# Kernel optimization log

Hardware: AMD Instinct MI355X
Metric: run time of the kernel (lower is better)

The kernel has to match this reference:

```python
import jax, jax.numpy as jnp
import numpy as np

B, C, H, W = 8, 256, 64, 64   # batch, num_hiddens, spatial
N, D = 1024, 256              # n_embed, embedding_dim
TEMP = 1.0                    # temp_init


def setup_inputs() -> dict:
    key = jax.random.key(0)
    k1, k2, k3 = jax.random.split(key, 3)
    z = jax.random.normal(k1, (B, C, H, W), dtype=jnp.float32)
    # 1x1 conv == per-pixel linear: weight [n_embed, num_hiddens], bias [n_embed]
    proj_w = jax.random.normal(k2, (N, C), dtype=jnp.float32) * 0.02
    proj_b = jnp.zeros((N,), dtype=jnp.float32)
    embed = jax.random.normal(k3, (N, D), dtype=jnp.float32) * 0.02
    return {"z": z, "proj_w": proj_w, "proj_b": proj_b, "embed": embed}


def reference(z, proj_w, proj_b, embed):
    # logits = Conv2d(num_hiddens, n_embed, 1)(z)  -> [b, n, h, w]
    logits = jnp.einsum('bchw,nc->bnhw', z, proj_w) + proj_b[None, :, None, None]
    # argmax_softmax (straight-through) over the codebook axis (dim=1), tau=TEMP
    y_soft = jax.nn.softmax(logits / TEMP, axis=1)
    ind = jnp.argmax(y_soft, axis=1)  # [b, h, w]
    y_hard = jax.nn.one_hot(ind, N, axis=1, dtype=logits.dtype)  # [b, n, h, w]
    soft_one_hot = y_hard - jax.lax.stop_gradient(y_soft) + y_soft
    # z_q = einsum('b n h w, n d -> b d h w', soft_one_hot, embed)
    z_q = jnp.einsum('bnhw,nd->bdhw', soft_one_hot, embed)
    diff = jnp.zeros((1,), dtype=logits.dtype)
    return (z_q, diff, ind)
```

## Files before the change

### kernel.cpp

```cpp
#include <hip/hip_runtime.h>
#include <math.h>

#define HWP 4096
#define CCH 256
#define NN  1024
#define DD  256
#define ZQ_SIZE (8 * DD * HWP)
#define MARGIN 1e-4f
#define WLCAP 4096

typedef _Float16 h8 __attribute__((ext_vector_type(8)));
typedef float    f4 __attribute__((ext_vector_type(4)));

__global__ __launch_bounds__(256) void split_w_k(
    const float* __restrict__ w, _Float16* __restrict__ whS, _Float16* __restrict__ wlS,
    int* __restrict__ wcount)
{
    if (blockIdx.x == 0 && threadIdx.x == 0) *wcount = 0;
    const int t = blockIdx.x * 256 + threadIdx.x;
    const int l = t & 63;
    const int frag = t >> 6;
    const int kc = frag & 7, r16 = frag >> 3;
    const int row = r16 * 16 + (l & 15);
    const int c   = kc * 32 + (l >> 4) * 8;
    const float* src = w + (size_t)row * CCH + c;
    _Float16 hv[8], lv[8];
#pragma unroll
    for (int j = 0; j < 8; ++j) {
        const float x = src[j];
        const _Float16 h = (_Float16)x;
        hv[j] = h;
        lv[j] = (_Float16)(x - (float)h);
    }
    *(h8*)(whS + (size_t)t * 8) = *(const h8*)hv;
    *(h8*)(wlS + (size_t)t * 8) = *(const h8*)lv;
}

__global__ __launch_bounds__(256) void split_zt_k(
    const float* __restrict__ z, _Float16* __restrict__ zhS, _Float16* __restrict__ zlS)
{
    __shared__ float t[64][68];
    const int tid = threadIdx.x;
    const int pt  = blockIdx.x >> 2;
    const int ct  = blockIdx.x & 3;
    const int b   = pt >> 6;
    const int p0  = (pt & 63) << 6;
    const int c0  = ct << 6;
    const float* zb = z + ((size_t)b * CCH + c0) * HWP + p0;
    {
        const int px4 = tid & 15, cr = tid >> 4;
#pragma unroll
        for (int it = 0; it < 4; ++it) {
            const int c = it * 16 + cr;
            const float4 v = *(const float4*)(zb + (size_t)c * HWP + px4 * 4);
            *(float4*)&t[c][px4 * 4] = v;
        }
    }
    __syncthreads();
    {
        const int c8 = tid & 7, pxl = tid >> 3;
#pragma unroll
        for (int it = 0; it < 2; ++it) {
            const int px = it * 32 + pxl;
            _Float16 hv[8], lv[8];
#pragma unroll
            for (int i = 0; i < 8; ++i) {
                const float x = t[c8 * 8 + i][px];
                const _Float16 h = (_Float16)x;
                hv[i] = h;
                lv[i] = (_Float16)(x - (float)h);
            }
            const int pxg  = pt * 64 + px;
            const int p16  = pxg >> 4;
            const int kc   = ct * 2 + (c8 >> 2);
            const int lane = (pxg & 15) + 16 * (c8 & 3);
            const size_t off = (((size_t)p16 * 8 + kc) * 64 + lane) * 8;
            *(h8*)(zhS + off) = *(const h8*)hv;
            *(h8*)(zlS + off) = *(const h8*)lv;
        }
    }
}

__global__ __launch_bounds__(256, 2) void mfma_gemm_k(
    const _Float16* __restrict__ zhS, const _Float16* __restrict__ zlS,
    const _Float16* __restrict__ whS, const _Float16* __restrict__ wlS,
    const float* __restrict__ bias,
    unsigned short* __restrict__ idx16, int* __restrict__ wcount,
    int* __restrict__ wlist, float* __restrict__ out)
{
    __shared__ float s_best[4][64];
    __shared__ float s_sec [4][64];
    __shared__ int   s_idx [4][64];

    const int tid = threadIdx.x;
    const int l   = tid & 63;
    const int wv  = tid >> 6;
    const int c15 = l & 15, g = l >> 4;
    const int pix0  = blockIdx.x * 64;
    const int p16_0 = blockIdx.x * 4;

    float best[16], sec[16]; int bidx[16];
#pragma unroll
    for (int s = 0; s < 16; ++s) { best[s] = -INFINITY; sec[s] = -INFINITY; bidx[s] = 0; }

#pragma unroll 1
    for (int nt = 0; nt < 4; ++nt) {
        const int n0 = nt * 256 + wv * 64;
        const int r16_0 = n0 >> 4;
        f4 acc[4][4];
#pragma unroll
        for (int mf = 0; mf < 4; ++mf)
#pragma unroll
            for (int nf = 0; nf < 4; ++nf) acc[mf][nf] = (f4)0.f;

#pragma unroll 2
        for (int kc = 0; kc < 8; ++kc) {
            h8 ah[4], al[4], bh[4], bl[4];
#pragma unroll
            for (int mf = 0; mf < 4; ++mf) {
                const size_t ao = (((size_t)(p16_0 + mf) * 8 + kc) * 64 + l) * 8;
                ah[mf] = *(const h8*)(zhS + ao);
                al[mf] = *(const h8*)(zlS + ao);
            }
#pragma unroll
            for (int nf = 0; nf < 4; ++nf) {
                const size_t bo = (((size_t)(r16_0 + nf) * 8 + kc) * 64 + l) * 8;
                bh[nf] = *(const h8*)(whS + bo);
                bl[nf] = *(const h8*)(wlS + bo);
            }
#pragma unroll
            for (int mf = 0; mf < 4; ++mf)
#pragma unroll
                for (int nf = 0; nf < 4; ++nf) {
                    acc[mf][nf] = __builtin_amdgcn_mfma_f32_16x16x32_f16(ah[mf], bh[nf], acc[mf][nf], 0, 0, 0);
                    acc[mf][nf] = __builtin_amdgcn_mfma_f32_16x16x32_f16(ah[mf], bl[nf], acc[mf][nf], 0, 0, 0);
                    acc[mf][nf] = __builtin_amdgcn_mfma_f32_16x16x32_f16(al[mf], bh[nf], acc[mf][nf], 0, 0, 0);
                }
        }
#pragma unroll
        for (int nf = 0; nf < 4; ++nf) {
            const int n_abs = n0 + nf * 16 + c15;
            const float bv = bias[n_abs];
#pragma unroll
            for (int mf = 0; mf < 4; ++mf)
#pragma unroll
                for (int r = 0; r < 4; ++r) {
                    const float v = acc[mf][nf][r] + bv;
                    const int s = mf * 4 + r;
                    if (v > best[s]) { sec[s] = best[s]; best[s] = v; bidx[s] = n_abs; }
                    else if (v > sec[s]) sec[s] = v;
                }
        }
    }

#pragma unroll
    for (int d = 1; d < 16; d <<= 1) {
#pragma unroll
        for (int s = 0; s < 16; ++s) {
            const float ob = __shfl_xor(best[s], d, 64);
            const float os = __shfl_xor(sec[s], d, 64);
            const int   oi = __shfl_xor(bidx[s], d, 64);
            if (ob > best[s])       { sec[s] = fmaxf(best[s], os); best[s] = ob; bidx[s] = oi; }
            else if (ob == best[s]) { sec[s] = ob; bidx[s] = (oi < bidx[s]) ? oi : bidx[s]; }
            else                    { sec[s] = fmaxf(sec[s], ob); }
        }
    }
#pragma unroll
    for (int s = 0; s < 16; ++s) {
        if (c15 == s) {
            const int px = (s >> 2) * 16 + g * 4 + (s & 3);
            s_best[wv][px] = best[s];
            s_sec [wv][px] = sec[s];
            s_idx [wv][px] = bidx[s];
        }
    }
    __syncthreads();
    if (tid < 64) {
        float b0 = s_best[0][tid], s0 = s_sec[0][tid]; int i0 = s_idx[0][tid];
#pragma unroll
        for (int c = 1; c < 4; ++c) {
            const float ob = s_best[c][tid], os = s_sec[c][tid];
            const int   oi = s_idx[c][tid];
            if (ob > b0 || (ob == b0 && oi < i0)) { s0 = fmaxf(b0, os); b0 = ob; i0 = oi; }
            else                                  { s0 = fmaxf(s0, ob); }
        }
        const int pix = pix0 + tid;
        idx16[pix] = (unsigned short)i0;
        out[ZQ_SIZE + 1 + pix] = (float)i0;
        if (b0 - s0 < MARGIN) {
            const int pos = atomicAdd(wcount, 1);
            if (pos < WLCAP) wlist[pos] = pix;
        }
    }
    if (blockIdx.x == 0 && tid == 0) out[ZQ_SIZE] = 0.0f;
}

__global__ __launch_bounds__(256) void fixup_k(
    const float* __restrict__ z, const float* __restrict__ w,
    const float* __restrict__ bias,
    const int* __restrict__ wcount, const int* __restrict__ wlist,
    unsigned short* __restrict__ idx16, float* __restrict__ out)
{
    __shared__ float zsh[256];
    __shared__ float m_v[4];
    __shared__ int   m_i[4];

    const int tid = threadIdx.x;
    const int l = tid & 63, wv = tid >> 6;
    const int c15 = l & 15, q = l >> 4;
    int nw = *wcount;
    if (nw > WLCAP) nw = WLCAP;

    for (int e = blockIdx.x; e < nw; e += 256) {
        const int pix = wlist[e];
        const int b = pix >> 12, p = pix & 4095;
        __syncthreads();
        zsh[tid] = z[((size_t)b * CCH + tid) * HWP + p];
        __syncthreads();

        float best = -INFINITY; int bi = 0;
        for (int g16 = 0; g16 < 16; ++g16) {
            const int row = wv * 256 + g16 * 16 + c15;
            const float* wr = w + (size_t)row * CCH + q * 64;
            float part = 0.f;
#pragma unroll
            for (int j = 0; j < 16; ++j) {
                const float4 w4 = *(const float4*)(wr + j * 4);
                const float4 z4 = *(const float4*)&zsh[q * 64 + j * 4];
                part = fmaf(w4.x, z4.x, part);
                part = fmaf(w4.y, z4.y, part);
                part = fmaf(w4.z, z4.z, part);
                part = fmaf(w4.w, z4.w, part);
            }
            part += __shfl_xor(part, 16, 64);
            part += __shfl_xor(part, 32, 64);
            const float v = part + bias[row];
            if (v > best) { best = v; bi = row; }
        }
#pragma unroll
        for (int d = 1; d < 16; d <<= 1) {
            const float ob = __shfl_xor(best, d, 64);
            const int   oi = __shfl_xor(bi, d, 64);
            if (ob > best || (ob == best && oi < bi)) { best = ob; bi = oi; }
        }
        if (l == 0) { m_v[wv] = best; m_i[wv] = bi; }
        __syncthreads();
        if (tid == 0) {
            float v = m_v[0]; int i = m_i[0];
#pragma unroll
            for (int t = 1; t < 4; ++t)
                if (m_v[t] > v || (m_v[t] == v && m_i[t] < i)) { v = m_v[t]; i = m_i[t]; }
            idx16[pix] = (unsigned short)i;
            out[ZQ_SIZE + 1 + pix] = (float)i;
        }
    }
}

__global__ __launch_bounds__(256) void gather_k(
    const float* __restrict__ embed, const unsigned short* __restrict__ idx16,
    float* __restrict__ out)
{
    __shared__ __align__(16) float tile[64][257];
    __shared__ int indsh[64];

    const int tid = threadIdx.x;
    const int blk = blockIdx.x;
    const int b = blk >> 6, p0 = (blk & 63) << 6;
    const int pix0 = blk * 64;

    if (tid < 64) indsh[tid] = (int)idx16[pix0 + tid];
    __syncthreads();

    const int lq = tid & 63, wq = tid >> 6;
    for (int it = 0; it < 16; ++it) {
        const int p   = it * 4 + wq;
        const int row = indsh[p];
        const float4 e = *(const float4*)(embed + (size_t)row * DD + lq * 4);
        tile[p][lq * 4 + 0] = e.x;
        tile[p][lq * 4 + 1] = e.y;
        tile[p][lq * 4 + 2] = e.z;
        tile[p][lq * 4 + 3] = e.w;
    }
    __syncthreads();
    float* outz = out + (size_t)b * DD * HWP + p0;
    for (int dd = 0; dd < 64; ++dd) {
        const int d = dd * 4 + wq;
        outz[(size_t)d * HWP + lq] = tile[lq][d];
    }
}

extern "C" void kernel_launch(void* const* d_in, const int* in_sizes, int n_in,
                              void* d_out, int out_size, void* d_ws, size_t ws_size,
                              hipStream_t stream) {
    const float* z     = (const float*)d_in[0];
    const float* w     = (const float*)d_in[1];
    const float* bias  = (const float*)d_in[2];
    const float* embed = (const float*)d_in[3];
    float* out = (float*)d_out;

    _Float16* whS = (_Float16*)d_ws;
    _Float16* wlS = (_Float16*)((char*)d_ws + 524288);
    unsigned short* idx16 = (unsigned short*)((char*)d_ws + 1048576);
    int* wcount = (int*)((char*)d_ws + 1114112);
    int* wlist  = (int*)((char*)d_ws + 1114368);

    _Float16* zhS = (_Float16*)d_out;
    _Float16* zlS = (_Float16*)((char*)d_out + 16777216);

    hipLaunchKernelGGL(split_w_k,   dim3(128),  dim3(256), 0, stream, w, whS, wlS, wcount);
    hipLaunchKernelGGL(split_zt_k,  dim3(2048), dim3(256), 0, stream, z, zhS, zlS);
    hipLaunchKernelGGL(mfma_gemm_k, dim3(512),  dim3(256), 0, stream,
                       zhS, zlS, whS, wlS, bias, idx16, wcount, wlist, out);
    hipLaunchKernelGGL(fixup_k,     dim3(256),  dim3(256), 0, stream,
                       z, w, bias, wcount, wlist, idx16, out);
    hipLaunchKernelGGL(gather_k,    dim3(512),  dim3(256), 0, stream,
                       embed, idx16, out);
}
```

Measured before the change: 216.1 us.

## Fuse z split/transposition and embedding gather into the MFMA argmax kernel

Removes the separate split_zt kernel by having each GEMM block load its own 64 pixels of z, split them into fp16 hi/lo, and stage them in LDS. It also removes gather_k by writing the embedding rows for each block's pixels straight from the GEMM kernel through an LDS tile. The fixup kernel now rewrites the z_q column for corrected pixels. This avoids global round-trips for the split z and the index array and saves two launches. In exchange the GEMM kernel uses about 68KB of LDS, which may reduce occupancy, and its z loads are strided scalar reads.

```diff
diff --git a/kernel.cpp b/kernel.cpp
--- a/kernel.cpp
+++ b/kernel.cpp
@@ -36,68 +36,52 @@
     *(h8*)(wlS + (size_t)t * 8) = *(const h8*)lv;
 }
 
-__global__ __launch_bounds__(256) void split_zt_k(
-    const float* __restrict__ z, _Float16* __restrict__ zhS, _Float16* __restrict__ zlS)
+__global__ __launch_bounds__(256, 2) void mfma_gemm_k(
+    const float* __restrict__ z,
+    const _Float16* __restrict__ whS, const _Float16* __restrict__ wlS,
+    const float* __restrict__ bias, const float* __restrict__ embed,
+    int* __restrict__ wcount, int* __restrict__ wlist,
+    float* __restrict__ out)
 {
-    __shared__ float t[64][68];
-    const int tid = threadIdx.x;
-    const int pt  = blockIdx.x >> 2;
-    const int ct  = blockIdx.x & 3;
-    const int b   = pt >> 6;
-    const int p0  = (pt & 63) << 6;
-    const int c0  = ct << 6;
-    const float* zb = z + ((size_t)b * CCH + c0) * HWP + p0;
-    {
-        const int px4 = tid & 15, cr = tid >> 4;
-#pragma unroll
-        for (int it = 0; it < 4; ++it) {
-            const int c = it * 16 + cr;
-            const float4 v = *(const float4*)(zb + (size_t)c * HWP + px4 * 4);
-            *(float4*)&t[c][px4 * 4] = v;
-        }
-    }
-    __syncthreads();
-    {
-        const int c8 = tid & 7, pxl = tid >> 3;
-#pragma unroll
-        for (int it = 0; it < 2; ++it) {
-            const int px = it * 32 + pxl;
-            _Float16 hv[8], lv[8];
-#pragma unroll
-            for (int i = 0; i < 8; ++i) {
-                const float x = t[c8 * 8 + i][px];
-                const _Float16 h = (_Float16)x;
-                hv[i] = h;
-                lv[i] = (_Float16)(x - (float)h);
-            }
-            const int pxg  = pt * 64 + px;
-            const int p16  = pxg >> 4;
-            const int kc   = ct * 2 + (c8 >> 2);
-            const int lane = (pxg & 15) + 16 * (c8 & 3);
-            const size_t off = (((size_t)p16 * 8 + kc) * 64 + lane) * 8;
-            *(h8*)(zhS + off) = *(const h8*)hv;
-            *(h8*)(zlS + off) = *(const h8*)lv;
-        }
-    }
-}
-
-__global__ __launch_bounds__(256, 2) void mfma_gemm_k(
-    const _Float16* __restrict__ zhS, const _Float16* __restrict__ zlS,
-    const _Float16* __restrict__ whS, const _Float16* __restrict__ wlS,
-    const float* __restrict__ bias,
-    unsigned short* __restrict__ idx16, int* __restrict__ wcount,
-    int* __restrict__ wlist, float* __restrict__ out)
-{
-    __shared__ float s_best[4][64];
-    __shared__ float s_sec [4][64];
-    __shared__ int   s_idx [4][64];
+    __shared__ __align__(16) char smem[68608];
+    __shared__ int indsh2[64];
+    float* s_best = (float*)(smem + 65536);
+    float* s_sec  = (float*)(smem + 66560);
+    int*   s_idx  = (int*)  (smem + 67584);
 
     const int tid = threadIdx.x;
     const int l   = tid & 63;
     const int wv  = tid >> 6;
     const int c15 = l & 15, g = l >> 4;
-    const int pix0  = blockIdx.x * 64;
-    const int p16_0 = blockIdx.x * 4;
+    const int pix0 = blockIdx.x * 64;
+    const int b = pix0 >> 12, p0 = pix0 & 4095;
+
+    {
+        const int px = tid & 63;
+        const int p16 = px >> 4;
+        const float* zb = z + (size_t)b * CCH * HWP + p0 + px;
+#pragma unroll
+        for (int it = 0; it < 8; ++it) {
+            const int cg = wv * 8 + it;
+            const int c = cg * 8;
+            float xv[8];
+#pragma unroll
+            for (int i = 0; i < 8; ++i) xv[i] = zb[(size_t)(c + i) * HWP];
+            _Float16 hv[8], lv[8];
+#pragma unroll
+            for (int i = 0; i < 8; ++i) {
+                const _Float16 h = (_Float16)xv[i];
+                hv[i] = h;
+                lv[i] = (_Float16)(xv[i] - (float)h);
+            }
+            const int kc = cg >> 2;
+            const int lane = (px & 15) + 16 * (cg & 3);
+            const int off = ((p16 * 8 + kc) * 64 + lane) * 16;
+            *(h8*)(smem + off)         = *(const h8*)hv;
+            *(h8*)(smem + 32768 + off) = *(const h8*)lv;
+        }
+    }
+    __syncthreads();
 
     float best[16], sec[16]; int bidx[16];
 #pragma unroll
@@ -118,9 +102,9 @@
             h8 ah[4], al[4], bh[4], bl[4];
 #pragma unroll
             for (int mf = 0; mf < 4; ++mf) {
-                const size_t ao = (((size_t)(p16_0 + mf) * 8 + kc) * 64 + l) * 8;
-                ah[mf] = *(const h8*)(zhS + ao);
-                al[mf] = *(const h8*)(zlS + ao);
+                const int ao = ((mf * 8 + kc) * 64 + l) * 16;
+                ah[mf] = *(const h8*)(smem + ao);
+                al[mf] = *(const h8*)(smem + 32768 + ao);
             }
 #pragma unroll
             for (int nf = 0; nf < 4; ++nf) {
@@ -169,23 +153,23 @@
     for (int s = 0; s < 16; ++s) {
         if (c15 == s) {
             const int px = (s >> 2) * 16 + g * 4 + (s & 3);
-            s_best[wv][px] = best[s];
-            s_sec [wv][px] = sec[s];
-            s_idx [wv][px] = bidx[s];
+            s_best[wv * 64 + px] = best[s];
+            s_sec [wv * 64 + px] = sec[s];
+            s_idx [wv * 64 + px] = bidx[s];
         }
     }
     __syncthreads();
     if (tid < 64) {
-        float b0 = s_best[0][tid], s0 = s_sec[0][tid]; int i0 = s_idx[0][tid];
+        float b0 = s_best[tid], s0 = s_sec[tid]; int i0 = s_idx[tid];
 #pragma unroll
         for (int c = 1; c < 4; ++c) {
-            const float ob = s_best[c][tid], os = s_sec[c][tid];
-            const int   oi = s_idx[c][tid];
+            const float ob = s_best[c * 64 + tid], os = s_sec[c * 64 + tid];
+            const int   oi = s_idx[c * 64 + tid];
             if (ob > b0 || (ob == b0 && oi < i0)) { s0 = fmaxf(b0, os); b0 = ob; i0 = oi; }
             else                                  { s0 = fmaxf(s0, ob); }
         }
         const int pix = pix0 + tid;
-        idx16[pix] = (unsigned short)i0;
+        indsh2[tid] = i0;
         out[ZQ_SIZE + 1 + pix] = (float)i0;
         if (b0 - s0 < MARGIN) {
             const int pos = atomicAdd(wcount, 1);
@@ -193,17 +177,44 @@
         }
     }
     if (blockIdx.x == 0 && tid == 0) out[ZQ_SIZE] = 0.0f;
+    __syncthreads();
+
+    float (*tile)[257] = (float (*)[257])smem;
+    const int lq = tid & 63, wq = tid >> 6;
+    const int l32 = tid & 31, dq = tid >> 5;
+#pragma unroll 1
+    for (int pp = 0; pp < 2; ++pp) {
+#pragma unroll
+        for (int it = 0; it < 8; ++it) {
+            const int pl = it * 4 + wq;
+            const int row = indsh2[pp * 32 + pl];
+            const float4 e = *(const float4*)(embed + (size_t)row * DD + lq * 4);
+            tile[pl][lq * 4 + 0] = e.x;
+            tile[pl][lq * 4 + 1] = e.y;
+            tile[pl][lq * 4 + 2] = e.z;
+            tile[pl][lq * 4 + 3] = e.w;
+        }
+        __syncthreads();
+        float* outz = out + (size_t)b * DD * HWP + p0 + pp * 32;
+#pragma unroll
+        for (int dd = 0; dd < 32; ++dd) {
+            const int d = dd * 8 + dq;
+            outz[(size_t)d * HWP + l32] = tile[l32][d];
+        }
+        __syncthreads();
+    }
 }
 
 __global__ __launch_bounds__(256) void fixup_k(
     const float* __restrict__ z, const float* __restrict__ w,
-    const float* __restrict__ bias,
+    const float* __restrict__ bias, const float* __restrict__ embed,
     const int* __restrict__ wcount, const int* __restrict__ wlist,
-    unsigned short* __restrict__ idx16, float* __restrict__ out)
+    float* __restrict__ out)
 {
     __shared__ float zsh[256];
     __shared__ float m_v[4];
     __shared__ int   m_i[4];
+    __shared__ int   s_i;
 
     const int tid = threadIdx.x;
     const int l = tid & 63, wv = tid >> 6;
@@ -250,42 +261,12 @@
 #pragma unroll
             for (int t = 1; t < 4; ++t)
                 if (m_v[t] > v || (m_v[t] == v && m_i[t] < i)) { v = m_v[t]; i = m_i[t]; }
-            idx16[pix] = (unsigned short)i;
+            s_i = i;
             out[ZQ_SIZE + 1 + pix] = (float)i;
         }
-    }
-}
-
-__global__ __launch_bounds__(256) void gather_k(
-    const float* __restrict__ embed, const unsigned short* __restrict__ idx16,
-    float* __restrict__ out)
-{
-    __shared__ __align__(16) float tile[64][257];
-    __shared__ int indsh[64];
-
-    const int tid = threadIdx.x;
-    const int blk = blockIdx.x;
-    const int b = blk >> 6, p0 = (blk & 63) << 6;
-    const int pix0 = blk * 64;
-
-    if (tid < 64) indsh[tid] = (int)idx16[pix0 + tid];
-    __syncthreads();
-
-    const int lq = tid & 63, wq = tid >> 6;
-    for (int it = 0; it < 16; ++it) {
-        const int p   = it * 4 + wq;
-        const int row = indsh[p];
-        const float4 e = *(const float4*)(embed + (size_t)row * DD + lq * 4);
-        tile[p][lq * 4 + 0] = e.x;
-        tile[p][lq * 4 + 1] = e.y;
-        tile[p][lq * 4 + 2] = e.z;
-        tile[p][lq * 4 + 3] = e.w;
-    }
-    __syncthreads();
-    float* outz = out + (size_t)b * DD * HWP + p0;
-    for (int dd = 0; dd < 64; ++dd) {
-        const int d = dd * 4 + wq;
-        outz[(size_t)d * HWP + lq] = tile[lq][d];
+        __syncthreads();
+        const int ii = s_i;
+        out[((size_t)b * DD + tid) * HWP + p] = embed[(size_t)ii * DD + tid];
     }
 }
 
@@ -300,19 +281,12 @@
 
     _Float16* whS = (_Float16*)d_ws;
     _Float16* wlS = (_Float16*)((char*)d_ws + 524288);
-    unsigned short* idx16 = (unsigned short*)((char*)d_ws + 1048576);
-    int* wcount = (int*)((char*)d_ws + 1114112);
-    int* wlist  = (int*)((char*)d_ws + 1114368);
-
-    _Float16* zhS = (_Float16*)d_out;
-    _Float16* zlS = (_Float16*)((char*)d_out + 16777216);
-
-    hipLaunchKernelGGL(split_w_k,   dim3(128),  dim3(256), 0, stream, w, whS, wlS, wcount);
-    hipLaunchKernelGGL(split_zt_k,  dim3(2048), dim3(256), 0, stream, z, zhS, zlS);
-    hipLaunchKernelGGL(mfma_gemm_k, dim3(512),  dim3(256), 0, stream,
-                       zhS, zlS, whS, wlS, bias, idx16, wcount, wlist, out);
-    hipLaunchKernelGGL(fixup_k,     dim3(256),  dim3(256), 0, stream,
-                       z, w, bias, wcount, wlist, idx16, out);
-    hipLaunchKernelGGL(gather_k,    dim3(512),  dim3(256), 0, stream,
-                       embed, idx16, out);
-}
+    int* wcount = (int*)((char*)d_ws + 1048576);
+    int* wlist  = (int*)((char*)d_ws + 1048832);
+
+    hipLaunchKernelGGL(split_w_k,   dim3(128), dim3(256), 0, stream, w, whS, wlS, wcount);
+    hipLaunchKernelGGL(mfma_gemm_k, dim3(512), dim3(256), 0, stream,
+                       z, whS, wlS, bias, embed, wcount, wlist, out);
+    hipLaunchKernelGGL(fixup_k,     dim3(256), dim3(256), 0, stream,
+                       z, w, bias, embed, wcount, wlist, out);
+}
```

Measured after the change: 186.0 us. -14.0%, faster.
